# Optimization experiments

Measured on AMD Instinct MI355X. Metric: run time of the kernel, lower is better.

Reference implementation:

```python
import jax, jax.numpy as jnp
import numpy as np

B, T, DEMO, V, NMOD = 64, 4096, 8, 1, 15
NPOS = 16                      # n_positional_dims
PHI_IN = NPOS + V + NMOD       # 32
PHI_W, LAT = 128, 128
PSI_W, PSI_LAT = 128, 128
DP, H = 64, 4                  # dot_prod_dim, n_heads
RHO_W, OUT = 128, 1
MAX_TIMESCALE = 100.0


def _he(k, din, dout):
    return jax.random.normal(k, (din, dout), jnp.float32) * np.sqrt(2.0 / din)


def setup_inputs() -> dict:
    key = jax.random.key(0)
    ks = jax.random.split(key, 24)
    inp = {
        'demo': jax.random.normal(ks[0], (B, DEMO), jnp.float32),
        'times': jax.random.uniform(ks[1], (B, T, 1), jnp.float32) * 100.0,
        'values': jax.random.normal(ks[2], (B, T, V), jnp.float32),
        'measurements': jax.random.randint(ks[3], (B, T), 0, NMOD),
        'lengths': jax.random.randint(ks[4], (B,), 1, T),
    }
    i = [5]
    def nd(din, dout):
        w = _he(ks[i[0]], din, dout); i[0] += 1
        return w, jnp.zeros((dout,), jnp.float32)
    p = {}
    p['demo_w1'], p['demo_b1'] = nd(DEMO, PHI_W)
    p['demo_w2'], p['demo_b2'] = nd(PHI_W, PHI_IN)
    p['phi_w1'], p['phi_b1'] = nd(PHI_IN, PHI_W)
    p['phi_w2'], p['phi_b2'] = nd(PHI_W, PHI_W)
    p['phi_w3'], p['phi_b3'] = nd(PHI_W, LAT)
    p['psi_w1'], p['psi_b1'] = nd(PHI_IN, PSI_W)
    p['psi_w2'], p['psi_b2'] = nd(PSI_W, PSI_W)
    p['psi_w3'], p['psi_b3'] = nd(PSI_W, PSI_LAT)
    p['rho_attn_w'], p['rho_attn_b'] = nd(PSI_LAT, LAT)
    p['W_k'] = _he(ks[i[0]], PHI_IN + LAT, DP * H); i[0] += 1
    p['W_q'] = jax.random.normal(ks[i[0]], (H, DP), jnp.float32) * 0.02; i[0] += 1
    p['rho_w1'], p['rho_b1'] = nd(H * LAT, RHO_W)
    p['rho_w2'], p['rho_b2'] = nd(RHO_W, RHO_W)
    p['rho_w3'], p['rho_b3'] = nd(RHO_W, OUT)
    inp.update(p)
    return inp


def reference(demo, times, values, measurements, lengths,
              demo_w1, demo_b1, demo_w2, demo_b2,
              phi_w1, phi_b1, phi_w2, phi_b2, phi_w3, phi_b3,
              psi_w1, psi_b1, psi_w2, psi_b2, psi_w3, psi_b3,
              rho_attn_w, rho_attn_b, W_k, W_q,
              rho_w1, rho_b1, rho_w2, rho_b2, rho_w3, rho_b3):
    relu = jax.nn.relu
    # positional encoding of observation times  [B,T,NPOS]
    timescales = MAX_TIMESCALE ** jnp.linspace(0.0, 1.0, NPOS // 2).astype(times.dtype)
    scaled = times / timescales[None, None, :]
    tt = jnp.concatenate([jnp.sin(scaled), jnp.cos(scaled)], axis=-1)
    onehot = jax.nn.one_hot(measurements, NMOD, dtype=tt.dtype)
    combined = jnp.concatenate([tt, values, onehot], axis=-1)        # [B,T,PHI_IN]
    # demographics encoder -> extra set element prepended per batch
    demo_enc = relu(demo @ demo_w1 + demo_b1) @ demo_w2 + demo_b2    # [B,PHI_IN]
    x = jnp.concatenate([demo_enc[:, None, :], combined], axis=1)    # [B,T+1,PHI_IN]
    mask = jnp.arange(T + 1)[None, :] < (lengths + 1)[:, None]       # [B,T+1]
    maskf = mask.astype(x.dtype)
    # phi network  [B,T+1,LAT]
    enc = relu(relu(relu(x @ phi_w1 + phi_b1) @ phi_w2 + phi_b2) @ phi_w3 + phi_b3)
    # attention psi network + segment (masked) mean
    psi = relu(relu(relu(x @ psi_w1 + psi_b1) @ psi_w2 + psi_b2) @ psi_w3 + psi_b3)
    cnt = jnp.sum(maskf, axis=1, keepdims=True)                      # [B,1]
    agg = jnp.sum(psi * maskf[..., None], axis=1) / cnt              # [B,PSI_LAT]
    agg = relu(agg @ rho_attn_w + rho_attn_b)                        # [B,LAT]
    comb = jnp.concatenate(
        [x, jnp.broadcast_to(agg[:, None, :], (B, T + 1, LAT))], axis=-1)
    keys = (comb @ W_k).reshape(B, T + 1, H, DP)
    preattn = jnp.einsum('bthd,hd->bth', keys, W_q) / jnp.sqrt(jnp.asarray(DP, x.dtype))
    preattn = jnp.where(mask[..., None], preattn, -1e9)
    attn = jax.nn.softmax(preattn, axis=1)                           # segment softmax [B,T+1,H]
    # per-head weighted segment sum, heads concatenated
    head_agg = jnp.einsum('bth,btl->bhl', attn, enc * maskf[..., None])
    feat = head_agg.reshape(B, H * LAT)
    out = relu(relu(feat @ rho_w1 + rho_b1) @ rho_w2 + rho_b2) @ rho_w3 + rho_b3
    return jax.nn.sigmoid(out)
```

## Files before the change

### kernel.cpp

```cpp
#include <hip/hip_runtime.h>
#include <math.h>

#define TT     4096
#define NTILE  65
#define NCHUNK (NTILE*64)
#define NWG    512
#define PREC   516
#define NB     64

typedef short s16x8 __attribute__((ext_vector_type(8)));
typedef float f32x4 __attribute__((ext_vector_type(4)));

__device__ __constant__ float INV_TS[8] = {
    1.0f,                 0.5179474679231213f, 0.2682695795279726f, 0.1389495494373138f,
    0.0719685673001152f,  0.0372759372031494f, 0.0193069772888325f, 0.01f };

__device__ __forceinline__ ushort f2bf(float f) {
    uint u = __float_as_uint(f);
    return (ushort)((u + 0x7fffu + ((u >> 16) & 1u)) >> 16);
}
__device__ __forceinline__ float bf2f(ushort h) {
    return __uint_as_float(((uint)h) << 16);
}
__device__ __forceinline__ uint pk2r(float a, float b) {
    return ((__float_as_uint(a) + 0x8000u) >> 16) |
           ((__float_as_uint(b) + 0x8000u) & 0xffff0000u);
}

__global__ __launch_bounds__(128) void prep_all(
    const float* __restrict__ demo,
    const float* __restrict__ dw1, const float* __restrict__ db1,
    const float* __restrict__ dw2, const float* __restrict__ db2,
    const float* __restrict__ W_k, const float* __restrict__ W_q,
    const float* __restrict__ w1, const float* __restrict__ w2,
    const float* __restrict__ w3,
    float* __restrict__ demo_enc, float* __restrict__ w_eff,
    ushort* __restrict__ ws16, float* __restrict__ partials)
{
    const int b = blockIdx.x, tid = threadIdx.x;
    if (b < NB) {
        for (int j = tid; j < PREC; j += 128) partials[b*PREC + j] = 0.f;
        __shared__ float h[128];
        float a = db1[tid];
#pragma unroll
        for (int k = 0; k < 8; k++) a += demo[b*8 + k] * dw1[k*128 + tid];
        h[tid] = fmaxf(a, 0.f);
        __syncthreads();
        if (tid < 32) {
            float e = db2[tid];
            for (int k = 0; k < 128; k++) e += h[k] * dw2[k*32 + tid];
            demo_enc[b*32 + tid] = e;
        }
    } else if (b == NB) {
        const int f = tid >> 2, hh = tid & 3;
        float s = 0.f;
        for (int d = 0; d < 64; d++) s += W_k[f*256 + hh*64 + d] * W_q[hh*64 + d];
        w_eff[f*4 + hh] = s * 0.125f;
    } else {
        ushort* w1T_hi = ws16;
        ushort* w2T_hi = ws16 + 8192;
        ushort* w2T_lo = w2T_hi + 16384;
        ushort* w3T_hi = w2T_lo + 16384;
        const int n = (b - 65) & 127, which = (b - 65) >> 7, k = tid;
        if (which == 0) {
            float v = w2[k*128 + n]; ushort h = f2bf(v);
            w2T_hi[n*128 + k] = h; w2T_lo[n*128 + k] = f2bf(v - bf2f(h));
        } else if (which == 1) {
            w3T_hi[n*128 + k] = f2bf(w3[k*128 + n]);
        } else if (k < 32) {
            w1T_hi[n*32 + k] = f2bf(w1[k*128 + n]);
        }
    }
}

__global__ __launch_bounds__(256, 2) void fused_main(
    const float* __restrict__ times,  const float* __restrict__ values,
    const int*   __restrict__ meas,   const int*   __restrict__ lengths,
    const float* __restrict__ demo_enc, const float* __restrict__ w_eff,
    const ushort* __restrict__ wT16,
    const float* __restrict__ b1, const float* __restrict__ b2,
    const float* __restrict__ b3,
    float* __restrict__ partials)
{
    const ushort* w1T_hi = wT16;
    const ushort* w2T_hi = wT16 + 8192;
    const ushort* w2T_lo = w2T_hi + 16384;
    const ushort* w3T_hi = w2T_lo + 16384;

    __shared__ ushort Xhi[64][40];
    __shared__ ushort Hhi[64][136];
    __shared__ ushort H2[64][136];
    __shared__ float  wexp[64][4];
    __shared__ float  spart[4][64][4];

    const int tid  = threadIdx.x;
    const int lane = tid & 63, wav = tid >> 6;
    const int l15  = lane & 15, q = lane >> 4;
    const int nb0  = wav * 32;
    const int t    = lane;

    s16x8 ah1[2];              f32x4 bv1[2];
    s16x8 ah2[2][4], al2[2][4]; f32x4 bv2[2];
    s16x8 wb3[2][4];           float b3l[2];
#pragma unroll
    for (int nt = 0; nt < 2; nt++) {
        const int np = nb0 + nt*16 + l15;
        ah1[nt] = *(const s16x8*)(w1T_hi + np*32 + q*8);
        bv1[nt] = *(const f32x4*)(b1 + nb0 + nt*16 + q*4);
#pragma unroll
        for (int ks = 0; ks < 4; ks++) {
            ah2[nt][ks] = *(const s16x8*)(w2T_hi + np*128 + ks*32 + q*8);
            al2[nt][ks] = *(const s16x8*)(w2T_lo + np*128 + ks*32 + q*8);
            wb3[nt][ks] = *(const s16x8*)(w3T_hi + np*128 + ks*32 + q*8);
        }
        bv2[nt] = *(const f32x4*)(b2 + nb0 + nt*16 + q*4);
        b3l[nt] = b3[np];
    }

    int c = blockIdx.x;
    float pf_tm = 0.f, pf_vl = 0.f; int pf_mm = -1;
    {
        const int bb = c / 65, gt = (c % 65) * 64 + t;
        if (gt >= 1 && gt <= TT) {
            const int ti = bb*TT + gt - 1;
            pf_tm = times[ti]; pf_vl = values[ti]; pf_mm = meas[ti];
        }
    }

#pragma unroll 1
    while (c < NCHUNK) {
        const int b = c / 65, tile = c % 65;
        const int gt = tile * 64 + t;
        const int len = lengths[b];

        float x[8];
        if (gt == 0) {
#pragma unroll
            for (int j = 0; j < 8; j++) x[j] = demo_enc[b*32 + wav*8 + j];
        } else if (gt <= TT) {
            if (wav == 0) {
#pragma unroll
                for (int j = 0; j < 8; j++) x[j] = sinf(pf_tm * INV_TS[j]);
            } else if (wav == 1) {
#pragma unroll
                for (int j = 0; j < 8; j++) x[j] = cosf(pf_tm * INV_TS[j]);
            } else if (wav == 2) {
                x[0] = pf_vl;
#pragma unroll
                for (int j = 1; j < 8; j++) x[j] = (pf_mm == j-1) ? 1.f : 0.f;
            } else {
#pragma unroll
                for (int j = 0; j < 8; j++) x[j] = (pf_mm == 7+j) ? 1.f : 0.f;
            }
        } else {
#pragma unroll
            for (int j = 0; j < 8; j++) x[j] = 0.f;
        }
        {
            float s0 = 0, s1 = 0, s2 = 0, s3 = 0;
#pragma unroll
            for (int j = 0; j < 8; j++) {
                const float* we = w_eff + (wav*8 + j)*4;
                s0 += x[j]*we[0]; s1 += x[j]*we[1]; s2 += x[j]*we[2]; s3 += x[j]*we[3];
            }
            f32x4 sv = {s0, s1, s2, s3};
            *(f32x4*)&spart[wav][t][0] = sv;
        }
        {
            uint4 uh = {pk2r(x[0],x[1]), pk2r(x[2],x[3]), pk2r(x[4],x[5]), pk2r(x[6],x[7])};
            *(uint4*)&Xhi[t][wav*8] = uh;
        }
        const int cn = c + NWG;
        if (cn < NCHUNK) {
            const int bb = cn / 65, gt2 = (cn % 65) * 64 + t;
            if (gt2 >= 1 && gt2 <= TT) {
                const int ti = bb*TT + gt2 - 1;
                pf_tm = times[ti]; pf_vl = values[ti]; pf_mm = meas[ti];
            } else { pf_mm = -1; }
        }
        __syncthreads();
        {
            float ss = spart[0][t][wav] + spart[1][t][wav]
                     + spart[2][t][wav] + spart[3][t][wav];
            wexp[t][wav] = (gt <= len) ? __expf(ss) : 0.f;
        }

#pragma unroll
        for (int tt = 0; tt < 4; tt++) {
            const int m = tt*16 + l15;
            s16x8 bh = *(const s16x8*)&Xhi[m][q*8];
#pragma unroll
            for (int nt = 0; nt < 2; nt++) {
                f32x4 acc = {0.f, 0.f, 0.f, 0.f};
                acc = __builtin_amdgcn_mfma_f32_16x16x32_bf16(ah1[nt], bh, acc, 0, 0, 0);
                uint2 uh = {pk2r(fmaxf(acc[0]+bv1[nt][0],0.f), fmaxf(acc[1]+bv1[nt][1],0.f)),
                            pk2r(fmaxf(acc[2]+bv1[nt][2],0.f), fmaxf(acc[3]+bv1[nt][3],0.f))};
                *(uint2*)&Hhi[m][nb0 + nt*16 + q*4] = uh;
            }
        }
        __syncthreads();

#pragma unroll
        for (int tt = 0; tt < 4; tt++) {
            const int m = tt*16 + l15;
            s16x8 bh[4];
#pragma unroll
            for (int ks = 0; ks < 4; ks++) bh[ks] = *(const s16x8*)&Hhi[m][ks*32 + q*8];
#pragma unroll
            for (int nt = 0; nt < 2; nt++) {
                f32x4 acc = {0.f, 0.f, 0.f, 0.f};
#pragma unroll
                for (int ks = 0; ks < 4; ks++) {
                    acc = __builtin_amdgcn_mfma_f32_16x16x32_bf16(al2[nt][ks], bh[ks], acc, 0, 0, 0);
                    acc = __builtin_amdgcn_mfma_f32_16x16x32_bf16(ah2[nt][ks], bh[ks], acc, 0, 0, 0);
                }
                uint2 uh = {pk2r(fmaxf(acc[0]+bv2[nt][0],0.f), fmaxf(acc[1]+bv2[nt][1],0.f)),
                            pk2r(fmaxf(acc[2]+bv2[nt][2],0.f), fmaxf(acc[3]+bv2[nt][3],0.f))};
                *(uint2*)&H2[m][nb0 + nt*16 + q*4] = uh;
            }
        }
        __syncthreads();

        {
            float p2[2][4] = {{0.f,0.f,0.f,0.f},{0.f,0.f,0.f,0.f}};
            float zz[4]    = {0.f,0.f,0.f,0.f};
#pragma unroll
            for (int tt = 0; tt < 4; tt++) {
                const int m = tt*16 + l15;
                s16x8 a3[4];
#pragma unroll
                for (int ks = 0; ks < 4; ks++) a3[ks] = *(const s16x8*)&H2[m][ks*32 + q*8];
                f32x4 acc0 = {0.f,0.f,0.f,0.f}, acc1 = {0.f,0.f,0.f,0.f};
#pragma unroll
                for (int ks = 0; ks < 4; ks++) {
                    acc0 = __builtin_amdgcn_mfma_f32_16x16x32_bf16(a3[ks], wb3[0][ks], acc0, 0, 0, 0);
                    acc1 = __builtin_amdgcn_mfma_f32_16x16x32_bf16(a3[ks], wb3[1][ks], acc1, 0, 0, 0);
                }
#pragma unroll
                for (int r = 0; r < 4; r++) {
                    f32x4 w4 = *(const f32x4*)&wexp[tt*16 + q*4 + r][0];
                    float e0 = fmaxf(acc0[r] + b3l[0], 0.f);
                    float e1 = fmaxf(acc1[r] + b3l[1], 0.f);
#pragma unroll
                    for (int h = 0; h < 4; h++) {
                        p2[0][h] += w4[h] * e0;
                        p2[1][h] += w4[h] * e1;
                        zz[h]    += w4[h];
                    }
                }
            }
#pragma unroll
            for (int mask = 16; mask <= 32; mask <<= 1) {
#pragma unroll
                for (int nt = 0; nt < 2; nt++)
#pragma unroll
                    for (int h = 0; h < 4; h++) p2[nt][h] += __shfl_xor(p2[nt][h], mask);
#pragma unroll
                for (int h = 0; h < 4; h++) zz[h] += __shfl_xor(zz[h], mask);
            }
            float s0 = (q==0)?p2[0][0]:(q==1)?p2[0][1]:(q==2)?p2[0][2]:p2[0][3];
            float s1 = (q==0)?p2[1][0]:(q==1)?p2[1][1]:(q==2)?p2[1][2]:p2[1][3];
            float* outp = partials + (size_t)b * PREC;
            atomicAdd(&outp[q*128 + nb0 + l15],      s0);
            atomicAdd(&outp[q*128 + nb0 + 16 + l15], s1);
            if (wav == 0 && l15 == 0) {
                float sz = (q==0)?zz[0]:(q==1)?zz[1]:(q==2)?zz[2]:zz[3];
                atomicAdd(&outp[512 + q], sz);
            }
        }
        c = cn;
    }
}

__global__ __launch_bounds__(128) void final_kernel(
    const float* __restrict__ partials,
    const float* __restrict__ rw1, const float* __restrict__ rb1,
    const float* __restrict__ rw2, const float* __restrict__ rb2,
    const float* __restrict__ rw3, const float* __restrict__ rb3,
    float* __restrict__ out)
{
    const int b = blockIdx.x, tid = threadIdx.x;
    __shared__ float feat[512];
    __shared__ float r1s[128];
    __shared__ float r2s[128];
    __shared__ float zsh[4];
    const float* pb = partials + (size_t)b * PREC;
    if (tid < 4) zsh[tid] = pb[512 + tid];
    __syncthreads();
#pragma unroll
    for (int r = 0; r < 4; r++) {
        int o = tid + r*128;
        feat[o] = pb[o] / zsh[o >> 7];
    }
    __syncthreads();
    float a = rb1[tid];
    for (int k = 0; k < 512; k++) a += feat[k] * rw1[k*128 + tid];
    r1s[tid] = fmaxf(a, 0.f);
    __syncthreads();
    a = rb2[tid];
    for (int k = 0; k < 128; k++) a += r1s[k] * rw2[k*128 + tid];
    r2s[tid] = fmaxf(a, 0.f);
    __syncthreads();
    if (tid == 0) {
        float o = rb3[0];
        for (int k = 0; k < 128; k++) o += r2s[k] * rw3[k];
        out[b] = 1.f / (1.f + expf(-o));
    }
}

extern "C" void kernel_launch(void* const* d_in, const int* in_sizes, int n_in,
                              void* d_out, int out_size, void* d_ws, size_t ws_size,
                              hipStream_t stream) {
    const float* demo    = (const float*)d_in[0];
    const float* times   = (const float*)d_in[1];
    const float* values  = (const float*)d_in[2];
    const int*   meas    = (const int*)  d_in[3];
    const int*   lengths = (const int*)  d_in[4];
    const float* demo_w1 = (const float*)d_in[5];
    const float* demo_b1 = (const float*)d_in[6];
    const float* demo_w2 = (const float*)d_in[7];
    const float* demo_b2 = (const float*)d_in[8];
    const float* phi_w1  = (const float*)d_in[9];
    const float* phi_b1  = (const float*)d_in[10];
    const float* phi_w2  = (const float*)d_in[11];
    const float* phi_b2  = (const float*)d_in[12];
    const float* phi_w3  = (const float*)d_in[13];
    const float* phi_b3  = (const float*)d_in[14];
    const float* W_k     = (const float*)d_in[23];
    const float* W_q     = (const float*)d_in[24];
    const float* rho_w1  = (const float*)d_in[25];
    const float* rho_b1  = (const float*)d_in[26];
    const float* rho_w2  = (const float*)d_in[27];
    const float* rho_b2  = (const float*)d_in[28];
    const float* rho_w3  = (const float*)d_in[29];
    const float* rho_b3  = (const float*)d_in[30];

    float*  ws       = (float*)d_ws;
    float*  demo_enc = ws;
    float*  w_eff    = ws + 2048;
    ushort* wT16     = (ushort*)(ws + 2176);
    float*  partials = ws + 39040;

    prep_all<<<449, 128, 0, stream>>>(demo, demo_w1, demo_b1, demo_w2, demo_b2,
                                      W_k, W_q, phi_w1, phi_w2, phi_w3,
                                      demo_enc, w_eff, wT16, partials);
    fused_main<<<NWG, 256, 0, stream>>>(
        times, values, meas, lengths, demo_enc, w_eff, wT16,
        phi_b1, phi_b2, phi_b3, partials);
    final_kernel<<<NB, 128, 0, stream>>>(partials, rho_w1, rho_b1, rho_w2, rho_b2,
                                         rho_w3, rho_b3, (float*)d_out);
}
```

Before: 181.6 us.

## Compute attention-weighted head aggregation with MFMA via transposed LDS tiles

```diff
diff --git a/kernel.cpp b/kernel.cpp
--- a/kernel.cpp
+++ b/kernel.cpp
@@ -25,6 +25,9 @@
 __device__ __forceinline__ uint pk2r(float a, float b) {
     return ((__float_as_uint(a) + 0x8000u) >> 16) |
            ((__float_as_uint(b) + 0x8000u) & 0xffff0000u);
+}
+__device__ __forceinline__ ushort bfr(float a) {
+    return (ushort)((__float_as_uint(a) + 0x8000u) >> 16);
 }
 
 __global__ __launch_bounds__(128) void prep_all(
@@ -73,7 +76,9 @@
     }
 }
 
-__global__ __launch_bounds__(256, 2) void fused_main(
+__global__ void __launch_bounds__(256)
+__attribute__((amdgpu_waves_per_eu(2, 2)))
+fused_main(
     const float* __restrict__ times,  const float* __restrict__ values,
     const int*   __restrict__ meas,   const int*   __restrict__ lengths,
     const float* __restrict__ demo_enc, const float* __restrict__ w_eff,
@@ -90,8 +95,9 @@
     __shared__ ushort Xhi[64][40];
     __shared__ ushort Hhi[64][136];
     __shared__ ushort H2[64][136];
-    __shared__ float  wexp[64][4];
-    __shared__ float  spart[4][64][4];
+    __shared__ ushort encT[128][72];
+    __shared__ ushort wexpT[16][72];
+    __shared__ float  spart[4][4][64];
 
     const int tid  = threadIdx.x;
     const int lane = tid & 63, wav = tid >> 6;
@@ -99,9 +105,11 @@
     const int nb0  = wav * 32;
     const int t    = lane;
 
-    s16x8 ah1[2];              f32x4 bv1[2];
+    for (int i = tid; i < 12*36; i += 256) ((uint*)&wexpT[4][0])[i] = 0u;
+
+    s16x8 ah1[2];               f32x4 bv1[2];
     s16x8 ah2[2][4], al2[2][4]; f32x4 bv2[2];
-    s16x8 wb3[2][4];           float b3l[2];
+    s16x8 wb3[2][4];            float b3l[2];
 #pragma unroll
     for (int nt = 0; nt < 2; nt++) {
         const int np = nb0 + nt*16 + l15;
@@ -132,6 +140,7 @@
         const int b = c / 65, tile = c % 65;
         const int gt = tile * 64 + t;
         const int len = lengths[b];
+        float* outp = partials + (size_t)b * PREC;
 
         float x[8];
         if (gt == 0) {
@@ -140,10 +149,10 @@
         } else if (gt <= TT) {
             if (wav == 0) {
 #pragma unroll
-                for (int j = 0; j < 8; j++) x[j] = sinf(pf_tm * INV_TS[j]);
+                for (int j = 0; j < 8; j++) x[j] = __sinf(pf_tm * INV_TS[j]);
             } else if (wav == 1) {
 #pragma unroll
-                for (int j = 0; j < 8; j++) x[j] = cosf(pf_tm * INV_TS[j]);
+                for (int j = 0; j < 8; j++) x[j] = __cosf(pf_tm * INV_TS[j]);
             } else if (wav == 2) {
                 x[0] = pf_vl;
 #pragma unroll
@@ -163,8 +172,8 @@
                 const float* we = w_eff + (wav*8 + j)*4;
                 s0 += x[j]*we[0]; s1 += x[j]*we[1]; s2 += x[j]*we[2]; s3 += x[j]*we[3];
             }
-            f32x4 sv = {s0, s1, s2, s3};
-            *(f32x4*)&spart[wav][t][0] = sv;
+            spart[wav][0][t] = s0; spart[wav][1][t] = s1;
+            spart[wav][2][t] = s2; spart[wav][3][t] = s3;
         }
         {
             uint4 uh = {pk2r(x[0],x[1]), pk2r(x[2],x[3]), pk2r(x[4],x[5]), pk2r(x[6],x[7])};
@@ -180,9 +189,15 @@
         }
         __syncthreads();
         {
-            float ss = spart[0][t][wav] + spart[1][t][wav]
-                     + spart[2][t][wav] + spart[3][t][wav];
-            wexp[t][wav] = (gt <= len) ? __expf(ss) : 0.f;
+            float ss = spart[0][wav][t] + spart[1][wav][t]
+                     + spart[2][wav][t] + spart[3][wav][t];
+            float wxf = (gt <= len) ? __expf(ss) : 0.f;
+            ushort w16 = bfr(wxf);
+            wexpT[wav][t] = w16;
+            float wv = bf2f(w16);
+#pragma unroll
+            for (int mask = 1; mask <= 32; mask <<= 1) wv += __shfl_xor(wv, mask);
+            if (lane == 0) atomicAdd(&outp[512 + wav], wv);
         }
 
 #pragma unroll
@@ -221,51 +236,38 @@
         }
         __syncthreads();
 
+#pragma unroll
+        for (int tt = 0; tt < 4; tt++) {
+            const int m = tt*16 + l15;
+            s16x8 a3[4];
+#pragma unroll
+            for (int ks = 0; ks < 4; ks++) a3[ks] = *(const s16x8*)&H2[m][ks*32 + q*8];
+#pragma unroll
+            for (int nt = 0; nt < 2; nt++) {
+                f32x4 acc = {0.f,0.f,0.f,0.f};
+#pragma unroll
+                for (int ks = 0; ks < 4; ks++)
+                    acc = __builtin_amdgcn_mfma_f32_16x16x32_bf16(a3[ks], wb3[nt][ks], acc, 0, 0, 0);
+                uint2 uh = {pk2r(fmaxf(acc[0]+b3l[nt],0.f), fmaxf(acc[1]+b3l[nt],0.f)),
+                            pk2r(fmaxf(acc[2]+b3l[nt],0.f), fmaxf(acc[3]+b3l[nt],0.f))};
+                *(uint2*)&encT[nb0 + nt*16 + l15][tt*16 + q*4] = uh;
+            }
+        }
+
         {
-            float p2[2][4] = {{0.f,0.f,0.f,0.f},{0.f,0.f,0.f,0.f}};
-            float zz[4]    = {0.f,0.f,0.f,0.f};
-#pragma unroll
-            for (int tt = 0; tt < 4; tt++) {
-                const int m = tt*16 + l15;
-                s16x8 a3[4];
-#pragma unroll
-                for (int ks = 0; ks < 4; ks++) a3[ks] = *(const s16x8*)&H2[m][ks*32 + q*8];
-                f32x4 acc0 = {0.f,0.f,0.f,0.f}, acc1 = {0.f,0.f,0.f,0.f};
-#pragma unroll
-                for (int ks = 0; ks < 4; ks++) {
-                    acc0 = __builtin_amdgcn_mfma_f32_16x16x32_bf16(a3[ks], wb3[0][ks], acc0, 0, 0, 0);
-                    acc1 = __builtin_amdgcn_mfma_f32_16x16x32_bf16(a3[ks], wb3[1][ks], acc1, 0, 0, 0);
+            s16x8 af0 = *(const s16x8*)&wexpT[l15][q*8];
+            s16x8 af1 = *(const s16x8*)&wexpT[l15][32 + q*8];
+#pragma unroll
+            for (int nt = 0; nt < 2; nt++) {
+                const ushort* erow = &encT[nb0 + nt*16 + l15][0];
+                f32x4 hacc = {0.f,0.f,0.f,0.f};
+                hacc = __builtin_amdgcn_mfma_f32_16x16x32_bf16(af0, *(const s16x8*)(erow + q*8), hacc, 0, 0, 0);
+                hacc = __builtin_amdgcn_mfma_f32_16x16x32_bf16(af1, *(const s16x8*)(erow + 32 + q*8), hacc, 0, 0, 0);
+                if (q == 0) {
+#pragma unroll
+                    for (int r = 0; r < 4; r++)
+                        atomicAdd(&outp[r*128 + nb0 + nt*16 + l15], hacc[r]);
                 }
-#pragma unroll
-                for (int r = 0; r < 4; r++) {
-                    f32x4 w4 = *(const f32x4*)&wexp[tt*16 + q*4 + r][0];
-                    float e0 = fmaxf(acc0[r] + b3l[0], 0.f);
-                    float e1 = fmaxf(acc1[r] + b3l[1], 0.f);
-#pragma unroll
-                    for (int h = 0; h < 4; h++) {
-                        p2[0][h] += w4[h] * e0;
-                        p2[1][h] += w4[h] * e1;
-                        zz[h]    += w4[h];
-                    }
-                }
-            }
-#pragma unroll
-            for (int mask = 16; mask <= 32; mask <<= 1) {
-#pragma unroll
-                for (int nt = 0; nt < 2; nt++)
-#pragma unroll
-                    for (int h = 0; h < 4; h++) p2[nt][h] += __shfl_xor(p2[nt][h], mask);
-#pragma unroll
-                for (int h = 0; h < 4; h++) zz[h] += __shfl_xor(zz[h], mask);
-            }
-            float s0 = (q==0)?p2[0][0]:(q==1)?p2[0][1]:(q==2)?p2[0][2]:p2[0][3];
-            float s1 = (q==0)?p2[1][0]:(q==1)?p2[1][1]:(q==2)?p2[1][2]:p2[1][3];
-            float* outp = partials + (size_t)b * PREC;
-            atomicAdd(&outp[q*128 + nb0 + l15],      s0);
-            atomicAdd(&outp[q*128 + nb0 + 16 + l15], s1);
-            if (wav == 0 && l15 == 0) {
-                float sz = (q==0)?zz[0]:(q==1)?zz[1]:(q==2)?zz[2]:zz[3];
-                atomicAdd(&outp[512 + q], sz);
             }
         }
         c = cn;
```

After: 182.1 us. Within noise of the previous version (+0.2%).
